# Kernel tuning notes

Measured on AMD Instinct MI355X. Metric: run time of the kernel, lower is better.

Reference implementation:

```python
import jax, jax.numpy as jnp
import numpy as np

N = 100000      # nodes
E = 1600000     # directed edges (avg degree 16)
F_IN = 128      # n_features
D = 128         # embed_dim
OUT = 1         # out_features


def setup_inputs() -> dict:
    key = jax.random.key(0)
    ks = jax.random.split(key, 8)
    x = jax.random.normal(ks[0], (N, F_IN), dtype=jnp.float32)
    edge_index = jax.random.randint(ks[1], (2, E), 0, N, dtype=jnp.int64)
    # GCNConv weights (glorot-ish scale) and biases
    W1 = jax.random.normal(ks[2], (F_IN, D), dtype=jnp.float32) * (1.0 / np.sqrt(F_IN))
    b1 = jnp.zeros((D,), dtype=jnp.float32)
    W2 = jax.random.normal(ks[3], (D, D), dtype=jnp.float32) * (1.0 / np.sqrt(D))
    b2 = jnp.zeros((D,), dtype=jnp.float32)
    Wfc = jax.random.normal(ks[4], (D, OUT), dtype=jnp.float32) * (1.0 / np.sqrt(D))
    bfc = jnp.zeros((OUT,), dtype=jnp.float32)
    return {"x": x, "edge_index": edge_index, "W1": W1, "b1": b1,
            "W2": W2, "b2": b2, "Wfc": Wfc, "bfc": bfc}


def _gcn_conv(x, src, dst, W, b, n):
    """PyG GCNConv: h = X W; symmetric normalization with self-loops; scatter-add; + b."""
    h = x @ W                                  # [n, d] transform first
    loops = jnp.arange(n, dtype=src.dtype)
    s = jnp.concatenate([src, loops])          # self-loops appended
    d = jnp.concatenate([dst, loops])
    deg = jax.ops.segment_sum(jnp.ones_like(d, dtype=h.dtype), d, num_segments=n)
    dinv = jnp.where(deg > 0, jax.lax.rsqrt(deg), 0.0)
    norm = dinv[s] * dinv[d]                   # [E+n]
    msg = h[s] * norm[:, None]                 # gather + scale
    out = jax.ops.segment_sum(msg, d, num_segments=n)  # scatter-add to targets
    return out + b


def reference(x, edge_index, W1, b1, W2, b2, Wfc, bfc):
    src, dst = edge_index[0], edge_index[1]
    n = x.shape[0]
    h = jnp.tanh(_gcn_conv(x, src, dst, W1, b1, n))
    # F.dropout with training=False -> identity (eval mode)
    embeddings = jnp.tanh(_gcn_conv(h, src, dst, W2, b2, n))
    out = jax.nn.sigmoid(embeddings @ Wfc + bfc)
    return (out, embeddings)
```

## Files before the change

### kernel.cpp

```cpp
#include <hip/hip_runtime.h>
#include <math.h>

#define CAP 64
#define RNGB 8
#define RNG 256
#define MAXR 512
#define EPB 4096
#define PCAP 6144

typedef unsigned int uint;
typedef unsigned short ushort;
typedef __attribute__((ext_vector_type(8))) short bf16x8;
typedef __attribute__((ext_vector_type(4))) float f32x4;

__device__ __forceinline__ ushort f2bf(float f) {
  union { float f; uint u; } v; v.f = f;
  uint u = v.u;
  return (ushort)((u + 0x7fffu + ((u >> 16) & 1u)) >> 16);
}
__device__ __forceinline__ float bflo(uint p) {
  union { uint u; float f; } v; v.u = p << 16; return v.f;
}
__device__ __forceinline__ float bfhi(uint p) {
  union { uint u; float f; } v; v.u = p & 0xffff0000u; return v.f;
}
__device__ __forceinline__ uint pk2(float a, float b) {
  return (uint)f2bf(a) | ((uint)f2bf(b) << 16);
}
__device__ __forceinline__ uint pk2r(float a, float b, float& ra, float& rb) {
  ushort ha = f2bf(a), hb = f2bf(b);
  union { uint u; float f; } va, vb;
  va.u = (uint)ha << 16; vb.u = (uint)hb << 16;
  ra = a - va.f; rb = b - vb.f;
  return (uint)ha | ((uint)hb << 16);
}


__global__ __launch_bounds__(256) void k_partition(const int* __restrict__ src,
    const int* __restrict__ dst, int* __restrict__ cur,
    int2* __restrict__ part, int E, int nr) {
  __shared__ int lcnt[MAXR];
  __shared__ int basev[MAXR];
  const int t = threadIdx.x;
  const int b0 = blockIdx.x * EPB;
  for (int i = t; i < nr; i += 256) lcnt[i] = 0;
  __syncthreads();
  int es[16], ed[16], ko[16];
  #pragma unroll
  for (int j = 0; j < 16; ++j) {
    int e = b0 + j * 256 + t;
    int d = (e < E) ? dst[e] : -1;
    es[j] = (e < E) ? src[e] : 0;
    ed[j] = d;
    ko[j] = (d >= 0) ? atomicAdd(&lcnt[d >> RNGB], 1) : 0;
  }
  __syncthreads();
  for (int i = t; i < nr; i += 256) basev[i] = atomicAdd(cur + i, lcnt[i]);
  __syncthreads();
  #pragma unroll
  for (int j = 0; j < 16; ++j) {
    int d = ed[j];
    if (d >= 0) {
      int r = d >> RNGB;
      int off = basev[r] + ko[j];
      if (off < PCAP) part[(size_t)r * PCAP + off] = make_int2(es[j], d);
    }
  }
}


__global__ __launch_bounds__(256) void k_sortbkt(const int2* __restrict__ part,
    const int* __restrict__ cur, int* __restrict__ cnt, int* __restrict__ bucket,
    float* __restrict__ dinv, const float* __restrict__ W2, uint* __restrict__ Wp, int n) {
  __shared__ int lc[RNG];
  const int r = blockIdx.x;
  const int t = threadIdx.x;
  lc[t] = 0;
  if (r < 32) {
    int idx = r * 256 + t;
    int k2 = idx >> 7, col = idx & 127;
    Wp[idx] = pk2(W2[k2 * 256 + col], W2[k2 * 256 + 128 + col]);
  }
  __syncthreads();
  const int base = r << RNGB;
  const int cE = min(cur[r], PCAP);
  const int2* p = part + (size_t)r * PCAP;
  #pragma unroll 4
  for (int e = t; e < cE; e += 256) {
    int2 pe = p[e];
    int k = atomicAdd(&lc[pe.y - base], 1);
    if (k < CAP) bucket[(size_t)pe.y * CAP + k] = pe.x;
  }
  __syncthreads();
  int node = base + t;
  if (node < n) {
    int c = lc[t];
    cnt[node] = c;
    dinv[node] = rsqrtf((float)c + 1.0f);
  }
}


__global__ __launch_bounds__(256) void k_gemm_mfma(const float* __restrict__ X,
    const float* __restrict__ W, const float* __restrict__ dinv,
    ushort* __restrict__ H, int n, int ntiles) {
  const int lane = threadIdx.x & 63;
  const int quad = lane >> 4;
  const int sub  = lane & 15;
  const int wid    = (blockIdx.x * 256 + threadIdx.x) >> 6;
  const int nwaves = (gridDim.x * 256) >> 6;

  union { bf16x8 v; uint u[4]; } Bh[4][8];
  #pragma unroll
  for (int ki = 0; ki < 4; ++ki) {
    #pragma unroll
    for (int ct = 0; ct < 8; ++ct) {
      const float* wp = W + (ki * 32 + quad * 8) * 128 + ct * 16 + sub;
      Bh[ki][ct].u[0] = pk2(wp[0],   wp[128]);
      Bh[ki][ct].u[1] = pk2(wp[256], wp[384]);
      Bh[ki][ct].u[2] = pk2(wp[512], wp[640]);
      Bh[ki][ct].u[3] = pk2(wp[768], wp[896]);
    }
  }

  for (int tile = wid; tile < ntiles; tile += nwaves) {
    int base = tile * 16;
    int row  = base + sub;
    if (row >= n) row = n - 1;
    const float* xp = X + (size_t)row * 128 + quad * 8;

    f32x4 acc[8];
    #pragma unroll
    for (int ct = 0; ct < 8; ++ct) acc[ct] = (f32x4){0.f, 0.f, 0.f, 0.f};

    #pragma unroll
    for (int ki = 0; ki < 4; ++ki) {
      float4 xa = *(const float4*)(xp + ki * 32);
      float4 xb = *(const float4*)(xp + ki * 32 + 4);
      union { bf16x8 v; uint u[4]; } ah, al;
      float r0,r1,r2,r3,r4,r5,r6,r7;
      ah.u[0] = pk2r(xa.x, xa.y, r0, r1);
      ah.u[1] = pk2r(xa.z, xa.w, r2, r3);
      ah.u[2] = pk2r(xb.x, xb.y, r4, r5);
      ah.u[3] = pk2r(xb.z, xb.w, r6, r7);
      al.u[0] = pk2(r0, r1);
      al.u[1] = pk2(r2, r3);
      al.u[2] = pk2(r4, r5);
      al.u[3] = pk2(r6, r7);
      #pragma unroll
      for (int ct = 0; ct < 8; ++ct) {
        acc[ct] = __builtin_amdgcn_mfma_f32_16x16x32_bf16(ah.v, Bh[ki][ct].v, acc[ct], 0, 0, 0);
        acc[ct] = __builtin_amdgcn_mfma_f32_16x16x32_bf16(al.v, Bh[ki][ct].v, acc[ct], 0, 0, 0);
      }
    }

    float dv[4];
    #pragma unroll
    for (int r = 0; r < 4; ++r) {
      int rr = base + quad * 4 + r;
      dv[r] = (rr < n) ? dinv[rr] : 0.f;
    }
    #pragma unroll
    for (int ct = 0; ct < 8; ++ct) {
      #pragma unroll
      for (int r = 0; r < 4; ++r) {
        int rr = base + quad * 4 + r;
        if (rr < n)
          H[(size_t)rr * 128 + ct * 16 + sub] = f2bf(acc[ct][r] * dv[r]);
      }
    }
  }
}


__device__ __forceinline__ void acc8(float* a, uint4 v, bool act) {
  if (act) {
    a[0] += bflo(v.x); a[1] += bfhi(v.x); a[2] += bflo(v.y); a[3] += bfhi(v.y);
    a[4] += bflo(v.z); a[5] += bfhi(v.z); a[6] += bflo(v.w); a[7] += bfhi(v.w);
  }
}

__device__ __forceinline__ void gather8(const uint4* __restrict__ H4,
    const int* __restrict__ bk, int nc, int c, int cmax, int sub, float* a) {
  int i = 0;
  for (; i + 8 <= cmax; i += 8) {
    int4 sA = *(const int4*)(bk + i);
    int4 sB = *(const int4*)(bk + i + 4);
    int s0 = (i     < c) ? sA.x : nc;
    int s1 = (i + 1 < c) ? sA.y : nc;
    int s2 = (i + 2 < c) ? sA.z : nc;
    int s3 = (i + 3 < c) ? sA.w : nc;
    int s4 = (i + 4 < c) ? sB.x : nc;
    int s5 = (i + 5 < c) ? sB.y : nc;
    int s6 = (i + 6 < c) ? sB.z : nc;
    int s7 = (i + 7 < c) ? sB.w : nc;
    uint4 v0 = H4[(size_t)s0 * 16 + sub];
    uint4 v1 = H4[(size_t)s1 * 16 + sub];
    uint4 v2 = H4[(size_t)s2 * 16 + sub];
    uint4 v3 = H4[(size_t)s3 * 16 + sub];
    uint4 v4 = H4[(size_t)s4 * 16 + sub];
    uint4 v5 = H4[(size_t)s5 * 16 + sub];
    uint4 v6 = H4[(size_t)s6 * 16 + sub];
    uint4 v7 = H4[(size_t)s7 * 16 + sub];
    acc8(a, v0, i     < c); acc8(a, v1, i + 1 < c);
    acc8(a, v2, i + 2 < c); acc8(a, v3, i + 3 < c);
    acc8(a, v4, i + 4 < c); acc8(a, v5, i + 5 < c);
    acc8(a, v6, i + 6 < c); acc8(a, v7, i + 7 < c);
  }
  if (i + 4 <= cmax) {
    int4 sA = *(const int4*)(bk + i);
    int s0 = (i     < c) ? sA.x : nc;
    int s1 = (i + 1 < c) ? sA.y : nc;
    int s2 = (i + 2 < c) ? sA.z : nc;
    int s3 = (i + 3 < c) ? sA.w : nc;
    uint4 v0 = H4[(size_t)s0 * 16 + sub];
    uint4 v1 = H4[(size_t)s1 * 16 + sub];
    uint4 v2 = H4[(size_t)s2 * 16 + sub];
    uint4 v3 = H4[(size_t)s3 * 16 + sub];
    acc8(a, v0, i < c); acc8(a, v1, i + 1 < c);
    acc8(a, v2, i + 2 < c); acc8(a, v3, i + 3 < c);
    i += 4;
  }
  for (; i < cmax; ++i) {
    int s = (i < c) ? bk[i] : nc;
    uint4 v0 = H4[(size_t)s * 16 + sub];
    acc8(a, v0, i < c);
  }
}


template <bool FC>
__global__ __launch_bounds__(256, 6) void k_agg4(const ushort* __restrict__ H,
    const int* __restrict__ cnt, const int* __restrict__ bucket,
    const float* __restrict__ dinv, const float* __restrict__ bias,
    const float* __restrict__ Wfc, const float* __restrict__ bfc,
    float* __restrict__ OUT, float* __restrict__ OUTV, int n) {
  const int wave = (blockIdx.x * 256 + threadIdx.x) >> 6;
  const int lane = threadIdx.x & 63;
  const int sub = lane & 15;
  const int node = wave * 4 + (lane >> 4);
  const bool an = node < n;
  const int nc = an ? node : 0;
  const uint4* H4 = (const uint4*)H;

  uint4 v = H4[(size_t)nc * 16 + sub];
  float a[8] = {bflo(v.x),bfhi(v.x),bflo(v.y),bfhi(v.y),
                bflo(v.z),bfhi(v.z),bflo(v.w),bfhi(v.w)};
  int c = an ? min(cnt[nc], CAP) : 0;
  int cmax = max(c, __shfl_xor(c, 16)); cmax = max(cmax, __shfl_xor(cmax, 32));
  gather8(H4, bucket + (size_t)nc * CAP, nc, c, cmax, sub, a);

  float dn = an ? dinv[nc] : 0.f;
  float4 b0 = ((const float4*)bias)[sub * 2];
  float4 b1 = ((const float4*)bias)[sub * 2 + 1];
  float o[8];
  o[0] = tanhf(a[0]*dn + b0.x); o[1] = tanhf(a[1]*dn + b0.y);
  o[2] = tanhf(a[2]*dn + b0.z); o[3] = tanhf(a[3]*dn + b0.w);
  o[4] = tanhf(a[4]*dn + b1.x); o[5] = tanhf(a[5]*dn + b1.y);
  o[6] = tanhf(a[6]*dn + b1.z); o[7] = tanhf(a[7]*dn + b1.w);
  if (an) {
    float4* dst0 = (float4*)(OUT + (size_t)node * 128 + sub * 8);
    dst0[0] = make_float4(o[0], o[1], o[2], o[3]);
    dst0[1] = make_float4(o[4], o[5], o[6], o[7]);
  }
  if (FC) {
    float4 w0 = ((const float4*)Wfc)[sub * 2];
    float4 w1 = ((const float4*)Wfc)[sub * 2 + 1];
    float p = o[0]*w0.x + o[1]*w0.y + o[2]*w0.z + o[3]*w0.w
            + o[4]*w1.x + o[5]*w1.y + o[6]*w1.z + o[7]*w1.w;
    p += __shfl_down(p, 8, 16);
    p += __shfl_down(p, 4, 16);
    p += __shfl_down(p, 2, 16);
    p += __shfl_down(p, 1, 16);
    if (an && sub == 0) OUTV[node] = 1.0f / (1.0f + expf(-(p + bfc[0])));
  }
}


__global__ __launch_bounds__(256, 6) void k_agg_gemm(const ushort* __restrict__ H,
    const int* __restrict__ cnt, const int* __restrict__ bucket,
    const float* __restrict__ dinv, const float* __restrict__ bias,
    const uint* __restrict__ Wp, ushort* __restrict__ H2, int n) {
  __shared__ uint4 Lhi[16][17];
  __shared__ uint4 Llo[16][17];
  const int wid  = threadIdx.x >> 6;
  const int lane = threadIdx.x & 63;
  const int quad = lane >> 4, sub = lane & 15;
  const int trow = wid * 4 + quad;
  const int node = blockIdx.x * 16 + trow;
  const bool an = node < n;
  const int nc = an ? node : 0;
  const uint4* H4 = (const uint4*)H;

  uint4 v = H4[(size_t)nc * 16 + sub];
  float a[8] = {bflo(v.x),bfhi(v.x),bflo(v.y),bfhi(v.y),
                bflo(v.z),bfhi(v.z),bflo(v.w),bfhi(v.w)};
  int c = an ? min(cnt[nc], CAP) : 0;
  int cmax = max(c, __shfl_xor(c, 16)); cmax = max(cmax, __shfl_xor(cmax, 32));
  gather8(H4, bucket + (size_t)nc * CAP, nc, c, cmax, sub, a);

  float dn = an ? dinv[nc] : 0.f;
  float4 b0 = ((const float4*)bias)[sub * 2];
  float4 b1 = ((const float4*)bias)[sub * 2 + 1];
  float o0 = tanhf(a[0]*dn + b0.x), o1 = tanhf(a[1]*dn + b0.y);
  float o2 = tanhf(a[2]*dn + b0.z), o3 = tanhf(a[3]*dn + b0.w);
  float o4 = tanhf(a[4]*dn + b1.x), o5 = tanhf(a[5]*dn + b1.y);
  float o6 = tanhf(a[6]*dn + b1.z), o7 = tanhf(a[7]*dn + b1.w);

  union { uint u[4]; uint4 q; } ah, al;
  float r0,r1,r2,r3,r4,r5,r6,r7;
  ah.u[0] = pk2r(o0, o1, r0, r1);
  ah.u[1] = pk2r(o2, o3, r2, r3);
  ah.u[2] = pk2r(o4, o5, r4, r5);
  ah.u[3] = pk2r(o6, o7, r6, r7);
  al.u[0] = pk2(r0, r1);
  al.u[1] = pk2(r2, r3);
  al.u[2] = pk2(r4, r5);
  al.u[3] = pk2(r6, r7);
  Lhi[trow][sub] = ah.q;
  Llo[trow][sub] = al.q;
  __syncthreads();

  const int ct0 = wid * 2;
  union { bf16x8 v; uint u[4]; } B0[4], B1[4];
  #pragma unroll
  for (int ki = 0; ki < 4; ++ki) {
    #pragma unroll
    for (int j = 0; j < 4; ++j) {
      int krow = (ki * 16 + quad * 4 + j) * 128;
      B0[ki].u[j] = Wp[krow + ct0 * 16 + sub];
      B1[ki].u[j] = Wp[krow + (ct0 + 1) * 16 + sub];
    }
  }
  f32x4 acc0 = (f32x4){0.f,0.f,0.f,0.f};
  f32x4 acc1 = (f32x4){0.f,0.f,0.f,0.f};
  #pragma unroll
  for (int ki = 0; ki < 4; ++ki) {
    union { uint4 q; bf16x8 v; } Ah, Al;
    Ah.q = Lhi[sub][ki * 4 + quad];
    Al.q = Llo[sub][ki * 4 + quad];
    acc0 = __builtin_amdgcn_mfma_f32_16x16x32_bf16(Ah.v, B0[ki].v, acc0, 0, 0, 0);
    acc0 = __builtin_amdgcn_mfma_f32_16x16x32_bf16(Al.v, B0[ki].v, acc0, 0, 0, 0);
    acc1 = __builtin_amdgcn_mfma_f32_16x16x32_bf16(Ah.v, B1[ki].v, acc1, 0, 0, 0);
    acc1 = __builtin_amdgcn_mfma_f32_16x16x32_bf16(Al.v, B1[ki].v, acc1, 0, 0, 0);
  }
  const int base16 = blockIdx.x * 16;
  #pragma unroll
  for (int r = 0; r < 4; ++r) {
    int rr = base16 + quad * 4 + r;
    if (rr < n) {
      float dv = dinv[rr];
      H2[(size_t)rr * 128 + ct0 * 16 + sub]       = f2bf(acc0[r] * dv);
      H2[(size_t)rr * 128 + (ct0 + 1) * 16 + sub] = f2bf(acc1[r] * dv);
    }
  }
}


extern "C" void kernel_launch(void* const* d_in, const int* in_sizes, int n_in,
                              void* d_out, int out_size, void* d_ws, size_t ws_size,
                              hipStream_t stream) {
  const float* x   = (const float*)d_in[0];
  const int*   ei  = (const int*)d_in[1];
  const float* W1  = (const float*)d_in[2];
  const float* b1  = (const float*)d_in[3];
  const float* W2  = (const float*)d_in[4];
  const float* b2  = (const float*)d_in[5];
  const float* Wfc = (const float*)d_in[6];
  const float* bfc = (const float*)d_in[7];

  const int N = in_sizes[0] / 128;
  const int E = in_sizes[1] / 2;
  const int* src = ei;
  const int* dst = ei + E;
  const int nr = (N + RNG - 1) >> RNGB;

  float* out = (float*)d_out;
  float* emb = out + N;

  char* ws = (char*)d_ws;
  size_t used = 0;
  auto take = [&](size_t bytes) {
    char* p = ws + used; used += (bytes + 255) & ~(size_t)255; return p;
  };
  int*    cnt    = (int*)   take((size_t)N * 4);
  float*  dinv   = (float*) take((size_t)N * 4);
  int*    cur    = (int*)   take(MAXR * 4);
  uint*   Wp     = (uint*)  take(64 * 128 * 4);
  int*    bucket = (int*)   take((size_t)N * CAP * 4);
  ushort* bufH   = (ushort*)take((size_t)N * 128 * 2);
  size_t h2bytes = (((size_t)N * 128 * 2) + 255) & ~(size_t)255;
  bool fused = (used + h2bytes) <= ws_size;
  ushort* bufH2 = fused ? (ushort*)take((size_t)N * 128 * 2) : nullptr;
  int2*   part  = (int2*)bufH;

  const int ntiles = (N + 15) / 16;
  const int aggBlocks = (N + 15) / 16;

  hipMemsetAsync(cur, 0, MAXR * 4, stream);

  k_partition<<<(E + EPB - 1) / EPB, 256, 0, stream>>>(src, dst, cur, part, E, nr);
  k_sortbkt<<<nr, 256, 0, stream>>>(part, cur, cnt, bucket, dinv, W2, Wp, N);

  k_gemm_mfma<<<512, 256, 0, stream>>>(x, W1, dinv, bufH, N, ntiles);

  if (fused) {
    k_agg_gemm<<<aggBlocks, 256, 0, stream>>>(bufH, cnt, bucket, dinv, b1, Wp, bufH2, N);
    k_agg4<true><<<aggBlocks, 256, 0, stream>>>(bufH2, cnt, bucket, dinv, b2,
                                                Wfc, bfc, emb, out, N);
  } else {
    k_agg4<false><<<aggBlocks, 256, 0, stream>>>(bufH, cnt, bucket, dinv, b1,
                                                 nullptr, nullptr, emb, nullptr, N);
    k_gemm_mfma<<<512, 256, 0, stream>>>(emb, W2, dinv, bufH, N, ntiles);
    k_agg4<true><<<aggBlocks, 256, 0, stream>>>(bufH, cnt, bucket, dinv, b2,
                                                Wfc, bfc, emb, out, N);
  }
}
```

Before: 316.0 us.

## Pack partition edges into 32-bit words, stage writes in LDS, add nontemporal hints

The partition kernel now packs each edge as a 24-bit source index plus an 8-bit local destination in one word instead of an int2, halving partition traffic. It prefix-scans per-range counts in shared memory and stages edges so each range's global writes are contiguous and coalesced. Nontemporal loads and stores are added for bucket indices, counts, partition reads and the final embedding output to reduce cache pollution. The 24-bit packing assumes node indices below 2^24, and the added LDS staging lowers partition-kernel occupancy.

```diff
diff --git a/kernel.cpp b/kernel.cpp
--- a/kernel.cpp
+++ b/kernel.cpp
@@ -12,6 +12,7 @@
 typedef unsigned short ushort;
 typedef __attribute__((ext_vector_type(8))) short bf16x8;
 typedef __attribute__((ext_vector_type(4))) float f32x4;
+typedef __attribute__((ext_vector_type(4))) int i32x4;
 
 __device__ __forceinline__ ushort f2bf(float f) {
   union { float f; uint u; } v; v.f = f;
@@ -38,9 +39,13 @@
 
 __global__ __launch_bounds__(256) void k_partition(const int* __restrict__ src,
     const int* __restrict__ dst, int* __restrict__ cur,
-    int2* __restrict__ part, int E, int nr) {
+    uint* __restrict__ part, int E, int nr) {
   __shared__ int lcnt[MAXR];
+  __shared__ int lstart[MAXR];
   __shared__ int basev[MAXR];
+  __shared__ uint estage[EPB];
+  __shared__ ushort rstage[EPB];
+  __shared__ int nvalid_s;
   const int t = threadIdx.x;
   const int b0 = blockIdx.x * EPB;
   for (int i = t; i < nr; i += 256) lcnt[i] = 0;
@@ -55,21 +60,45 @@
     ko[j] = (d >= 0) ? atomicAdd(&lcnt[d >> RNGB], 1) : 0;
   }
   __syncthreads();
+  if (t < 64) {
+    int carry = 0;
+    for (int c = 0; c * 64 < nr; ++c) {
+      int idx = c * 64 + t;
+      int v = (idx < nr) ? lcnt[idx] : 0;
+      int sc = v;
+      #pragma unroll
+      for (int dsh = 1; dsh < 64; dsh <<= 1) {
+        int u = __shfl_up(sc, dsh);
+        if (t >= dsh) sc += u;
+      }
+      if (idx < nr) lstart[idx] = sc - v + carry;
+      carry += __shfl(sc, 63);
+    }
+    if (t == 0) nvalid_s = carry;
+  }
+  __syncthreads();
   for (int i = t; i < nr; i += 256) basev[i] = atomicAdd(cur + i, lcnt[i]);
-  __syncthreads();
   #pragma unroll
   for (int j = 0; j < 16; ++j) {
     int d = ed[j];
     if (d >= 0) {
       int r = d >> RNGB;
-      int off = basev[r] + ko[j];
-      if (off < PCAP) part[(size_t)r * PCAP + off] = make_int2(es[j], d);
-    }
-  }
-}
-
-
-__global__ __launch_bounds__(256) void k_sortbkt(const int2* __restrict__ part,
+      int slot = lstart[r] + ko[j];
+      estage[slot] = (uint)es[j] | ((uint)(d & (RNG - 1)) << 24);
+      rstage[slot] = (ushort)r;
+    }
+  }
+  __syncthreads();
+  const int nvalid = nvalid_s;
+  for (int i = t; i < nvalid; i += 256) {
+    int r = rstage[i];
+    int off = basev[r] + (i - lstart[r]);
+    if (off < PCAP) part[(size_t)r * PCAP + off] = estage[i];
+  }
+}
+
+
+__global__ __launch_bounds__(256) void k_sortbkt(const uint* __restrict__ part,
     const int* __restrict__ cur, int* __restrict__ cnt, int* __restrict__ bucket,
     float* __restrict__ dinv, const float* __restrict__ W2, uint* __restrict__ Wp, int n) {
   __shared__ int lc[RNG];
@@ -84,12 +113,14 @@
   __syncthreads();
   const int base = r << RNGB;
   const int cE = min(cur[r], PCAP);
-  const int2* p = part + (size_t)r * PCAP;
+  const uint* p = part + (size_t)r * PCAP;
   #pragma unroll 4
   for (int e = t; e < cE; e += 256) {
-    int2 pe = p[e];
-    int k = atomicAdd(&lc[pe.y - base], 1);
-    if (k < CAP) bucket[(size_t)pe.y * CAP + k] = pe.x;
+    uint pe = __builtin_nontemporal_load(p + e);
+    int dl = (int)(pe >> 24);
+    int s  = (int)(pe & 0xFFFFFFu);
+    int k = atomicAdd(&lc[dl], 1);
+    if (k < CAP) bucket[(size_t)(base + dl) * CAP + k] = s;
   }
   __syncthreads();
   int node = base + t;
@@ -184,8 +215,8 @@
     const int* __restrict__ bk, int nc, int c, int cmax, int sub, float* a) {
   int i = 0;
   for (; i + 8 <= cmax; i += 8) {
-    int4 sA = *(const int4*)(bk + i);
-    int4 sB = *(const int4*)(bk + i + 4);
+    i32x4 sA = __builtin_nontemporal_load((const i32x4*)(bk + i));
+    i32x4 sB = __builtin_nontemporal_load((const i32x4*)(bk + i + 4));
     int s0 = (i     < c) ? sA.x : nc;
     int s1 = (i + 1 < c) ? sA.y : nc;
     int s2 = (i + 2 < c) ? sA.z : nc;
@@ -208,7 +239,7 @@
     acc8(a, v6, i + 6 < c); acc8(a, v7, i + 7 < c);
   }
   if (i + 4 <= cmax) {
-    int4 sA = *(const int4*)(bk + i);
+    i32x4 sA = __builtin_nontemporal_load((const i32x4*)(bk + i));
     int s0 = (i     < c) ? sA.x : nc;
     int s1 = (i + 1 < c) ? sA.y : nc;
     int s2 = (i + 2 < c) ? sA.z : nc;
@@ -246,7 +277,7 @@
   uint4 v = H4[(size_t)nc * 16 + sub];
   float a[8] = {bflo(v.x),bfhi(v.x),bflo(v.y),bfhi(v.y),
                 bflo(v.z),bfhi(v.z),bflo(v.w),bfhi(v.w)};
-  int c = an ? min(cnt[nc], CAP) : 0;
+  int c = an ? min(__builtin_nontemporal_load(cnt + nc), CAP) : 0;
   int cmax = max(c, __shfl_xor(c, 16)); cmax = max(cmax, __shfl_xor(cmax, 32));
   gather8(H4, bucket + (size_t)nc * CAP, nc, c, cmax, sub, a);
 
@@ -259,9 +290,16 @@
   o[4] = tanhf(a[4]*dn + b1.x); o[5] = tanhf(a[5]*dn + b1.y);
   o[6] = tanhf(a[6]*dn + b1.z); o[7] = tanhf(a[7]*dn + b1.w);
   if (an) {
-    float4* dst0 = (float4*)(OUT + (size_t)node * 128 + sub * 8);
-    dst0[0] = make_float4(o[0], o[1], o[2], o[3]);
-    dst0[1] = make_float4(o[4], o[5], o[6], o[7]);
+    f32x4 w0 = { o[0], o[1], o[2], o[3] };
+    f32x4 w1 = { o[4], o[5], o[6], o[7] };
+    f32x4* dst0 = (f32x4*)(OUT + (size_t)node * 128 + sub * 8);
+    if (FC) {
+      __builtin_nontemporal_store(w0, dst0);
+      __builtin_nontemporal_store(w1, dst0 + 1);
+    } else {
+      dst0[0] = w0;
+      dst0[1] = w1;
+    }
   }
   if (FC) {
     float4 w0 = ((const float4*)Wfc)[sub * 2];
@@ -295,7 +333,7 @@
   uint4 v = H4[(size_t)nc * 16 + sub];
   float a[8] = {bflo(v.x),bfhi(v.x),bflo(v.y),bfhi(v.y),
                 bflo(v.z),bfhi(v.z),bflo(v.w),bfhi(v.w)};
-  int c = an ? min(cnt[nc], CAP) : 0;
+  int c = an ? min(__builtin_nontemporal_load(cnt + nc), CAP) : 0;
   int cmax = max(c, __shfl_xor(c, 16)); cmax = max(cmax, __shfl_xor(cmax, 32));
   gather8(H4, bucket + (size_t)nc * CAP, nc, c, cmax, sub, a);
 
@@ -392,7 +430,7 @@
   size_t h2bytes = (((size_t)N * 128 * 2) + 255) & ~(size_t)255;
   bool fused = (used + h2bytes) <= ws_size;
   ushort* bufH2 = fused ? (ushort*)take((size_t)N * 128 * 2) : nullptr;
-  int2*   part  = (int2*)bufH;
+  uint*   part  = (uint*)bufH;
 
   const int ntiles = (N + 15) / 16;
   const int aggBlocks = (N + 15) / 16;
```

Result: slower. 323.9 us (+2.5%).
